# Kernel tuning notes

Measured on AMD Instinct MI355X. Metric: run time of the kernel, lower is better.

## Reference

```python
import jax, jax.numpy as jnp
import numpy as np

N_NODES = 50000
N_EDGES = 800000
HIDDEN = 128
N_REL = 64
NUM_HEADS = 8
HEAD_DIM = HIDDEN // NUM_HEADS


def setup_inputs() -> dict:
    key = jax.random.key(0)
    ks = jax.random.split(key, 20)
    s = 0.05
    inp = {
        "x": jax.random.normal(ks[0], (N_NODES, HIDDEN), dtype=jnp.float32),
        "timestamps": jax.random.uniform(ks[1], (N_NODES,), dtype=jnp.float32),
        "src": jax.random.randint(ks[2], (N_EDGES,), 0, N_NODES),
        "dst": jax.random.randint(ks[3], (N_EDGES,), 0, N_NODES),
        "edge_type": jax.random.randint(ks[4], (N_EDGES,), 0, N_REL),
        "edge_time": jax.random.uniform(ks[5], (N_EDGES,), dtype=jnp.float32),
        # parameters (torch Linear stored as [in, out] so we use x @ W + b)
        "rel_table": jax.random.normal(ks[6], (N_REL, HIDDEN), dtype=jnp.float32) * s,
        "Wq": jax.random.normal(ks[7], (HIDDEN, HIDDEN), dtype=jnp.float32) * s,
        "bq": jnp.zeros((HIDDEN,), dtype=jnp.float32),
        "Wk": jax.random.normal(ks[8], (HIDDEN, HIDDEN), dtype=jnp.float32) * s,
        "bk": jnp.zeros((HIDDEN,), dtype=jnp.float32),
        "Wv": jax.random.normal(ks[9], (HIDDEN, HIDDEN), dtype=jnp.float32) * s,
        "bv": jnp.zeros((HIDDEN,), dtype=jnp.float32),
        "W1": jax.random.normal(ks[10], (2 * HIDDEN + 1, HIDDEN), dtype=jnp.float32) * s,
        "b1": jnp.zeros((HIDDEN,), dtype=jnp.float32),
        "W2": jax.random.normal(ks[11], (HIDDEN, 1), dtype=jnp.float32) * s,
        "b2": jnp.zeros((1,), dtype=jnp.float32),
        "time_coeff": jnp.array(1.0, dtype=jnp.float32),
    }
    return inp


def reference(x, timestamps, src, dst, edge_type, edge_time, rel_table,
              Wq, bq, Wk, bk, Wv, bv, W1, b1, W2, b2, time_coeff):
    N = x.shape[0]
    # temporal gating
    delta_t = (timestamps[dst] - edge_time) / (jnp.abs(time_coeff) + 1e-9)  # [E]
    time_mask = jax.nn.sigmoid(delta_t)[:, None]                            # [E,1]
    rel_emb = rel_table[edge_type] * time_mask                              # [E,H]
    src_emb = x[src]                                                        # [E,H]
    # dynamic edge weights: MLP([src_emb, rel_emb, time_mask]) -> sigmoid
    weight_input = jnp.concatenate([src_emb, rel_emb, time_mask], axis=-1)  # [E,2H+1]
    h = jax.nn.relu(weight_input @ W1 + b1)
    dynamic_weights = jax.nn.sigmoid(h @ W2 + b2)                           # [E,1]
    message = src_emb * rel_emb * dynamic_weights                           # [E,H]
    # multi-head edge attention keyed by dst
    q = (x[dst] @ Wq + bq).reshape(-1, NUM_HEADS, HEAD_DIM)
    k = (message @ Wk + bk).reshape(-1, NUM_HEADS, HEAD_DIM)
    v = (message @ Wv + bv).reshape(-1, NUM_HEADS, HEAD_DIM)
    scores = (q * k).sum(-1) / (HEAD_DIM ** 0.5)                            # [E,heads]
    # scatter softmax over edges grouped by dst
    seg_max = jax.ops.segment_max(scores, dst, num_segments=N)              # [N,heads]
    e = jnp.exp(scores - seg_max[dst])
    denom = jax.ops.segment_sum(e, dst, num_segments=N)
    attn = e / denom[dst]                                                   # [E,heads]
    out = jax.ops.segment_sum(v * attn[..., None], dst, num_segments=N)     # [N,heads,hd]
    return out.reshape(N, NUM_HEADS * HEAD_DIM)
```

## Files before the change

### kernel.cpp

```cpp
#include <hip/hip_runtime.h>

typedef __bf16 v8bf __attribute__((ext_vector_type(8)));
typedef __bf16 v4bf __attribute__((ext_vector_type(4)));
typedef float  v4f  __attribute__((ext_vector_type(4)));

#define MFMA16x16x32 __builtin_amdgcn_mfma_f32_16x16x32_bf16

#define HIDDEN 128
#define NHEADS 8

__global__ __launch_bounds__(512) void prep_all(
    const float* __restrict__ rel, const float* __restrict__ W1,
    const float* __restrict__ Wk, const float* __restrict__ Wv,
    const float* __restrict__ W2, const int* __restrict__ dst,
    int* __restrict__ count,
    __bf16* __restrict__ mlppre, __bf16* __restrict__ relbf,
    __bf16* __restrict__ wswz, __bf16* __restrict__ w2bf,
    float* __restrict__ outz,
    const float* __restrict__ x, const float* __restrict__ Wq,
    const float* __restrict__ bq, const float* __restrict__ b1,
    __bf16* __restrict__ qbf, __bf16* __restrict__ hpre, __bf16* __restrict__ xbf,
    int N, int E, int hb, int zb, int nz4)
{
  __shared__ __bf16 X[32][136];
  const int b = blockIdx.x;
  if (b < 64) {
    __shared__ float rrow[128];
    const int j = threadIdx.x;
    if (j < 128) rrow[j] = rel[b*HIDDEN + j];
    __syncthreads();
    if (j < 128) {
      float acc = W1[256*HIDDEN + j];
      #pragma unroll 4
      for (int k=0;k<128;k++) acc += rrow[k]*W1[(128+k)*HIDDEN + j];
      mlppre[b*HIDDEN + j] = (__bf16)acc;
      relbf [b*HIDDEN + j] = (__bf16)rrow[j];
    }
    return;
  }
  if (b < 72) {
    int f = (b - 64)*512 + threadIdx.x;
    if (f < 128) w2bf[f] = (__bf16)W2[f];
    if (f >= 2*8*4*64) return;
    int lane = f & 63, kk = (f>>6)&3, c = (f>>8)&7, mat = f>>11;
    const float* W = mat ? Wv : Wk;
    int qq = lane>>4, nn = lane&15;
    v8bf o;
    #pragma unroll
    for (int j=0;j<8;j++) o[j] = (__bf16)W[(kk*32 + qq*8 + j)*HIDDEN + c*16 + nn];
    *(v8bf*)(wswz + (long)f*8) = o;
    return;
  }
  if (b < 72 + hb) {
    long i = (long)(b - 72)*512 + threadIdx.x;
    long e4 = i*4;
    if (e4 + 3 < E) {
      int4 d = *(const int4*)(dst + e4);
      atomicAdd(&count[d.x], 1);
      atomicAdd(&count[d.y], 1);
      atomicAdd(&count[d.z], 1);
      atomicAdd(&count[d.w], 1);
    } else {
      for (long e = e4; e < E; e++) atomicAdd(&count[dst[e]], 1);
    }
    return;
  }
  if (b < 72 + hb + zb) {
    int idx = (b - 72 - hb)*512 + threadIdx.x;
    if (idx < nz4) ((float4*)outz)[idx] = make_float4(0.f,0.f,0.f,0.f);
    return;
  }
  const int pb = b - (72 + hb + zb), npb = gridDim.x - (72 + hb + zb);
  const int tid = threadIdx.x;
  const int w = tid >> 6, l = tid & 63, qd = l >> 4, ln = l & 15;
  const int col = w*16 + ln;

  v8bf BQ[4], BH[4];
  #pragma unroll
  for (int kk=0; kk<4; kk++) {
    v8bf f, g;
    #pragma unroll
    for (int j=0;j<8;j++){
      f[j] = (__bf16)Wq[(kk*32 + qd*8 + j)*HIDDEN + col];
      g[j] = (__bf16)W1[(kk*32 + qd*8 + j)*HIDDEN + col];
    }
    BQ[kk] = f; BH[kk] = g;
  }
  const float bqv = bq[col], b1v = b1[col];

  const int s = tid >> 4, c8 = (tid & 15)*8;
  for (int n0 = pb*32; n0 < N; n0 += npb*32) {
    __syncthreads();
    int n = n0 + s;
    v8bf xv;
    if (n < N) {
      const float4* xp = (const float4*)(x + (long)n*HIDDEN + c8);
      float4 a = xp[0], b2_ = xp[1];
      xv[0]=(__bf16)a.x; xv[1]=(__bf16)a.y; xv[2]=(__bf16)a.z; xv[3]=(__bf16)a.w;
      xv[4]=(__bf16)b2_.x; xv[5]=(__bf16)b2_.y; xv[6]=(__bf16)b2_.z; xv[7]=(__bf16)b2_.w;
      *(v8bf*)(xbf + (long)n*HIDDEN + c8) = xv;
    } else {
      #pragma unroll
      for (int j=0;j<8;j++) xv[j] = (__bf16)0.f;
    }
    *(v8bf*)&X[s][c8] = xv;
    __syncthreads();

    v4f q0={0.f,0.f,0.f,0.f}, q1={0.f,0.f,0.f,0.f};
    v4f h0={0.f,0.f,0.f,0.f}, h1={0.f,0.f,0.f,0.f};
    #pragma unroll
    for (int kk=0;kk<4;kk++) {
      v8bf a0 = *(const v8bf*)&X[ln][kk*32 + qd*8];
      v8bf a1 = *(const v8bf*)&X[16+ln][kk*32 + qd*8];
      q0 = MFMA16x16x32(a0, BQ[kk], q0, 0,0,0);
      q1 = MFMA16x16x32(a1, BQ[kk], q1, 0,0,0);
      h0 = MFMA16x16x32(a0, BH[kk], h0, 0,0,0);
      h1 = MFMA16x16x32(a1, BH[kk], h1, 0,0,0);
    }
    #pragma unroll
    for (int r=0;r<4;r++) {
      int n_o = n0 + qd*4 + r;
      if (n_o < N) {
        qbf [(long)n_o*HIDDEN + col] = (__bf16)(q0[r] + bqv);
        hpre[(long)n_o*HIDDEN + col] = (__bf16)(h0[r] + b1v);
      }
      int n2 = n0 + 16 + qd*4 + r;
      if (n2 < N) {
        qbf [(long)n2*HIDDEN + col] = (__bf16)(q1[r] + bqv);
        hpre[(long)n2*HIDDEN + col] = (__bf16)(h1[r] + b1v);
      }
    }
  }
}

__global__ __launch_bounds__(1024) void scan_kernel(const int* __restrict__ count,
    int* __restrict__ base, int N)
{
  __shared__ int ssum[1024];
  const int t = threadIdx.x;
  const int chunk = ((N + 4095) >> 12) << 2;
  const int lo = t*chunk, hi = min(lo + chunk, N);
  int s = 0;
  int i = lo;
  for (; i + 3 < hi; i += 4) {
    int4 v = *(const int4*)(count + i);
    s += v.x + v.y + v.z + v.w;
  }
  for (; i < hi; i++) s += count[i];
  ssum[t] = s;
  __syncthreads();
  #pragma unroll
  for (int ofs = 1; ofs < 1024; ofs <<= 1) {
    int v = (t >= ofs) ? ssum[t - ofs] : 0;
    __syncthreads();
    ssum[t] += v;
    __syncthreads();
  }
  int run = (t == 0) ? 0 : ssum[t-1];
  i = lo;
  for (; i + 3 < hi; i += 4) {
    int4 c = *(const int4*)(count + i);
    int4 o;
    o.x = run; o.y = run + c.x; o.z = o.y + c.y; o.w = o.z + c.z;
    *(int4*)(base + i) = o;
    run = o.w + c.w;
  }
  for (; i < hi; i++) { base[i] = run; run += count[i]; }
}

__global__ __launch_bounds__(512) void scat_dw(
    const int* __restrict__ src, const int* __restrict__ dstp,
    const int* __restrict__ etyp, const float* __restrict__ etime,
    const float* __restrict__ ts, const float* __restrict__ tc,
    const __bf16* __restrict__ hpre, const __bf16* __restrict__ mlppre,
    const __bf16* __restrict__ w2bf, const float* __restrict__ b2,
    const int* __restrict__ base, int* __restrict__ cursor,
    int4* __restrict__ meta4, int E)
{
  const int tid = threadIdx.x;
  const int wid = tid >> 6, l = tid & 63;
  const long e0 = ((long)blockIdx.x*8 + wid)*8;
  const int ei = l >> 3, lc = l & 7;

  int s_=0, d_=0, ty_=0; float et_=0.f, tsd_=0.f;
  if (l < 8 && e0 + l < E) {
    long e = e0 + l;
    s_ = src[e]; d_ = dstp[e]; ty_ = etyp[e]; et_ = etime[e]; tsd_ = ts[d_];
  }
  const int sE  = __shfl(s_, ei);
  const int dE  = __shfl(d_, ei);
  const int tyE = __shfl(ty_, ei);
  const float etE  = __shfl(et_, ei);
  const float tsdE = __shfl(tsd_, ei);

  const float invtc = 1.0f / (fabsf(tc[0]) + 1e-9f);
  const float dt = (tsdE - etE) * invtc;
  const float tm = 1.0f/(1.0f + __expf(-dt));

  const v8bf w2a = *(const v8bf*)(w2bf + lc*16);
  const v8bf w2b = *(const v8bf*)(w2bf + lc*16 + 8);
  const __bf16* hp = hpre  + (long)sE *HIDDEN + lc*16;
  const __bf16* mp = mlppre+ (long)tyE*HIDDEN + lc*16;
  v8bf av0 = *(const v8bf*)hp, av1 = *(const v8bf*)(hp + 8);
  v8bf bp0 = *(const v8bf*)mp, bp1 = *(const v8bf*)(mp + 8);

  float z = 0.f;
  #pragma unroll
  for (int j=0;j<8;j++){
    float p0 = (float)av0[j] + tm*(float)bp0[j];
    float p1 = (float)av1[j] + tm*(float)bp1[j];
    z += fmaxf(p0, 0.f)*(float)w2a[j] + fmaxf(p1, 0.f)*(float)w2b[j];
  }
  z += __shfl_xor(z,1); z += __shfl_xor(z,2); z += __shfl_xor(z,4);

  if (lc == 0 && e0 + ei < E) {
    float dw = 1.0f/(1.0f + __expf(-(z + b2[0])));
    int p = base[dE] + atomicAdd(&cursor[dE], 1);
    meta4[p] = make_int4(sE, dE, tyE, __float_as_int(tm * dw));
  }
}

__global__ __launch_bounds__(512, 4) void edge_fused6(
    const int4* __restrict__ meta4,
    const __bf16* __restrict__ xbf, const __bf16* __restrict__ qbf,
    const __bf16* __restrict__ relbf, const __bf16* __restrict__ wswz,
    const float* __restrict__ bk, const float* __restrict__ bv,
    float* __restrict__ out, float* __restrict__ denom, int E, int ntiles)
{
  __shared__ __align__(16) __bf16 MSG[2][4096];

  const int tid = threadIdx.x;
  const int wid = tid >> 6, l = tid & 63, qd = l >> 4, ln = l & 15;
  const int eIdx = wid*4 + qd;

  v8bf bkf[4], bvf[4];
  #pragma unroll
  for (int kk=0;kk<4;kk++){
    bkf[kk] = *(const v8bf*)(wswz +         wid*2048 + kk*512 + (size_t)l*8);
    bvf[kk] = *(const v8bf*)(wswz + 16384 + wid*2048 + kk*512 + (size_t)l*8);
  }
  const float bkc = bk[wid*16 + ln];
  const float bvc = bv[wid*16 + ln];

  const int G = gridDim.x;
  const int wg = ((int)blockIdx.x & 7)*(G >> 3) + ((int)blockIdx.x >> 3);
  const int lo = (int)((long)wg*ntiles/G);
  const int hi = (int)((long)(wg+1)*ntiles/G);
  if (lo >= hi) return;

  int t = lo;
  int4 mt = make_int4(0, -1, 0, 0);
  { int e = t*32 + l; if (l < 32 && e < E) mt = meta4[e]; }
  int tn = t + 1;
  int4 mtn = make_int4(0, -1, 0, 0);
  if (tn < hi) { int e = tn*32 + l; if (l < 32 && e < E) mtn = meta4[e]; }

  float sME = __int_as_float(__shfl(mt.w, eIdx));
  v8bf sv, rv;
  {
    int srcE = __shfl(mt.x, eIdx);
    int tyE  = __shfl(mt.z, eIdx);
    sv = *(const v8bf*)(xbf   + (long)srcE*HIDDEN + ln*8);
    rv = *(const v8bf*)(relbf + (long)tyE *HIDDEN + ln*8);
  }
  int dC[2][4];
  #pragma unroll
  for (int b=0;b<2;b++)
    #pragma unroll
    for (int r=0;r<4;r++) dC[b][r] = __shfl(mt.y, b*16 + qd*4 + r);
  float qA[2][4];
  #pragma unroll
  for (int b=0;b<2;b++)
    #pragma unroll
    for (int r=0;r<4;r++){
      int d = dC[b][r];
      qA[b][r] = (float)qbf[(long)(d<0?0:d)*HIDDEN + wid*16 + ln];
    }

  int p = 0;
  while (true) {
    const int d_m = mt.y;

    int dprev = __shfl(d_m, (l>0)?(l-1):0);
    int flag = (l < 32) && ((l==0) || (d_m != dprev));
    unsigned long long segmask = __ballot(flag);

    const int t2 = tn + 1;
    int4 mt2 = make_int4(0, -1, 0, 0);
    if (t2 < hi) { int e = t2*32 + l; if (l < 32 && e < E) mt2 = meta4[e]; }

    const float sMN = __int_as_float(__shfl(mtn.w, eIdx));
    const int srcN = __shfl(mtn.x, eIdx);
    const int tyN  = __shfl(mtn.z, eIdx);
    int dN[2][4];
    #pragma unroll
    for (int b=0;b<2;b++)
      #pragma unroll
      for (int r=0;r<4;r++) dN[b][r] = __shfl(mtn.y, b*16 + qd*4 + r);

    {
      char* wbase = (char*)&MSG[p][0] + eIdx*256;
      const int sw = (eIdx & 7) << 4;
      v8bf m;
      #pragma unroll
      for (int j=0;j<8;j++) m[j] = (__bf16)((float)sv[j]*(float)rv[j]*sME);
      *(v8bf*)(wbase + ((ln*16) ^ sw)) = m;
    }

    sv = *(const v8bf*)(xbf   + (long)srcN*HIDDEN + ln*8);
    rv = *(const v8bf*)(relbf + (long)tyN *HIDDEN + ln*8);

    float qB[2][4];
    #pragma unroll
    for (int b=0;b<2;b++)
      #pragma unroll
      for (int r=0;r<4;r++){
        int d = dN[b][r];
        qB[b][r] = (float)qbf[(long)(d<0?0:d)*HIDDEN + wid*16 + ln];
      }

    asm volatile("s_waitcnt lgkmcnt(0)" ::: "memory");
    __builtin_amdgcn_s_barrier();
    __builtin_amdgcn_sched_barrier(0);

    const char* rb = (const char*)&MSG[p][0];
    v4f aK[2], aV[2];
    __builtin_amdgcn_s_setprio(1);
    #pragma unroll
    for (int b=0;b<2;b++){
      const int rrow = b*16 + ln;
      const char* abase = rb + rrow*256;
      const int asw = (rrow & 7) << 4;
      v4f k_ = {0.f,0.f,0.f,0.f}, v_ = {0.f,0.f,0.f,0.f};
      #pragma unroll
      for (int kk=0;kk<4;kk++){
        v8bf a = *(const v8bf*)(abase + ((kk*64 + qd*16) ^ asw));
        k_ = MFMA16x16x32(a, bkf[kk], k_, 0,0,0);
        v_ = MFMA16x16x32(a, bvf[kk], v_, 0,0,0);
      }
      aK[b] = k_; aV[b] = v_;
    }
    __builtin_amdgcn_s_setprio(0);

    float sc[2][4];
    #pragma unroll
    for (int b=0;b<2;b++)
      #pragma unroll
      for (int r=0;r<4;r++) sc[b][r] = (aK[b][r] + bkc)*qA[b][r];
    #pragma unroll
    for (int m=1;m<16;m<<=1){
      #pragma unroll
      for (int b=0;b<2;b++)
        #pragma unroll
        for (int r=0;r<4;r++) sc[b][r] += __shfl_xor(sc[b][r], m);
    }
    float ee[2][4], wv[2][4];
    #pragma unroll
    for (int b=0;b<2;b++)
      #pragma unroll
      for (int r=0;r<4;r++){
        float e_ = __expf(sc[b][r]*0.25f);
        ee[b][r] = e_;
        wv[b][r] = e_*(aV[b][r] + bvc);
      }

    unsigned long long mm = segmask;
    while (mm){
      int s0 = __ffsll((long long)mm) - 1;
      mm &= mm - 1;
      int s1 = mm ? (__ffsll((long long)mm) - 1) : 32;
      int dseg = __shfl(d_m, s0);
      if (dseg < 0) continue;
      float a0 = 0.f, dn0 = 0.f;
      #pragma unroll
      for (int b=0;b<2;b++)
        #pragma unroll
        for (int r=0;r<4;r++){
          int rw = b*16 + qd*4 + r;
          bool in = (rw >= s0) && (rw < s1);
          a0  += in ? wv[b][r] : 0.f;
          dn0 += in ? ee[b][r] : 0.f;
        }
      a0  += __shfl_xor(a0,16);  a0  += __shfl_xor(a0,32);
      dn0 += __shfl_xor(dn0,16); dn0 += __shfl_xor(dn0,32);
      if (l < 16) atomicAdd(&out[(long)dseg*HIDDEN + wid*16 + ln], a0);
      if (l == 0) atomicAdd(&denom[(long)dseg*NHEADS + wid], dn0);
    }

    if (tn >= hi) break;
    t = tn; tn = t2; mt = mtn; mtn = mt2; sME = sMN;
    #pragma unroll
    for (int b=0;b<2;b++)
      #pragma unroll
      for (int r=0;r<4;r++){
        dC[b][r] = dN[b][r];
        qA[b][r] = qB[b][r];
      }
    p ^= 1;
  }
}

__global__ __launch_bounds__(512) void q_kernel(const float* __restrict__ x,
    const float* __restrict__ Wq, const float* __restrict__ bq,
    float* __restrict__ q, int N)
{
  __shared__ __bf16 X[32][136];
  const int tid = threadIdx.x;
  const int w = tid >> 6, l = tid & 63, qd = l >> 4, ln = l & 15;
  const int col = w*16 + ln;
  v8bf B[4];
  #pragma unroll
  for (int kk=0; kk<4; kk++) {
    v8bf f;
    #pragma unroll
    for (int j=0;j<8;j++) f[j] = (__bf16)Wq[(kk*32 + qd*8 + j)*HIDDEN + col];
    B[kk] = f;
  }
  const float bqv = bq[col];
  const int s = tid >> 4, c8 = (tid & 15)*8;
  for (int n0 = blockIdx.x*32; n0 < N; n0 += gridDim.x*32) {
    __syncthreads();
    int n = n0 + s;
    v8bf xv;
    if (n < N) {
      const float4* xp = (const float4*)(x + (long)n*HIDDEN + c8);
      float4 a = xp[0], b = xp[1];
      xv[0]=(__bf16)a.x; xv[1]=(__bf16)a.y; xv[2]=(__bf16)a.z; xv[3]=(__bf16)a.w;
      xv[4]=(__bf16)b.x; xv[5]=(__bf16)b.y; xv[6]=(__bf16)b.z; xv[7]=(__bf16)b.w;
    } else {
      #pragma unroll
      for (int j=0;j<8;j++) xv[j] = (__bf16)0.f;
    }
    *(v8bf*)&X[s][c8] = xv;
    __syncthreads();
    v4f acc0 = {0.f,0.f,0.f,0.f}, acc1 = {0.f,0.f,0.f,0.f};
    #pragma unroll
    for (int kk=0;kk<4;kk++) {
      v8bf a0 = *(const v8bf*)&X[ln][kk*32 + qd*8];
      v8bf a1 = *(const v8bf*)&X[16+ln][kk*32 + qd*8];
      acc0 = MFMA16x16x32(a0, B[kk], acc0, 0,0,0);
      acc1 = MFMA16x16x32(a1, B[kk], acc1, 0,0,0);
    }
    #pragma unroll
    for (int r=0;r<4;r++) {
      int n_o = n0 + qd*4 + r;
      if (n_o < N) q[(long)n_o*HIDDEN + col] = acc0[r] + bqv;
      int n_o2 = n0 + 16 + qd*4 + r;
      if (n_o2 < N) q[(long)n_o2*HIDDEN + col] = acc1[r] + bqv;
    }
  }
}

__global__ __launch_bounds__(512) void edge_atomic(
    const float* __restrict__ x, const float* __restrict__ ts,
    const int* __restrict__ src, const int* __restrict__ dst,
    const int* __restrict__ etyp, const float* __restrict__ etime,
    const float* __restrict__ rel,
    const float* __restrict__ Wk, const float* __restrict__ bk,
    const float* __restrict__ Wv, const float* __restrict__ bv,
    const float* __restrict__ W1, const float* __restrict__ b1,
    const float* __restrict__ W2, const float* __restrict__ b2,
    const float* __restrict__ tc,
    const float* __restrict__ qws, float* __restrict__ denom,
    float* __restrict__ out, int E)
{
  __shared__ __bf16 A[32][264];
  __shared__ __bf16 A2[32][136];
  __shared__ float sW2[128], sb1[128], sw1r[128], sbk[128], sbv[128];
  __shared__ float stm[32], sdw[32];
  __shared__ int   ssrc[32], sdst[32], styp[32];
  __shared__ float dwpart[8][32];
  const int tid = threadIdx.x;
  const int w = tid >> 6, l = tid & 63, qd = l >> 4, ln = l & 15;
  const int col = w*16 + ln;
  v8bf B1[8], BK[4], BV[4];
  #pragma unroll
  for (int kk=0;kk<8;kk++){ v8bf f;
    #pragma unroll
    for (int j=0;j<8;j++) f[j] = (__bf16)W1[(kk*32+qd*8+j)*HIDDEN + col];
    B1[kk]=f; }
  #pragma unroll
  for (int kk=0;kk<4;kk++){ v8bf f,g;
    #pragma unroll
    for (int j=0;j<8;j++){ f[j] = (__bf16)Wk[(kk*32+qd*8+j)*HIDDEN + col];
                           g[j] = (__bf16)Wv[(kk*32+qd*8+j)*HIDDEN + col]; }
    BK[kk]=f; BV[kk]=g; }
  if (tid < 128) {
    sW2[tid]=W2[tid]; sb1[tid]=b1[tid]; sw1r[tid]=W1[256*HIDDEN+tid];
    sbk[tid]=bk[tid]; sbv[tid]=bv[tid];
  }
  const float b2v = b2[0];
  const float invtc = 1.0f / (fabsf(tc[0]) + 1e-9f);
  const int s = tid >> 4, c8 = (tid & 15)*8;
  const int ntiles = (E + 31) >> 5;
  for (int t = blockIdx.x; t < ntiles; t += gridDim.x) {
    const int e0 = t*32;
    __syncthreads();
    if (tid < 32) {
      int e = e0 + tid;
      if (e < E) {
        int d = dst[e];
        ssrc[tid]=src[e]; sdst[tid]=d; styp[tid]=etyp[e];
        float dt = (ts[d] - etime[e]) * invtc;
        stm[tid] = 1.0f/(1.0f+expf(-dt));
      } else { ssrc[tid]=0; sdst[tid]=0; styp[tid]=0; stm[tid]=0.f; }
    }
    __syncthreads();
    {
      const float tmv = stm[s];
      const float4* xp = (const float4*)(x + (long)ssrc[s]*HIDDEN + c8);
      float4 a = xp[0], b = xp[1];
      const float4* rp = (const float4*)(rel + (long)styp[s]*HIDDEN + c8);
      float4 ra = rp[0], rb = rp[1];
      v8bf sv, rv;
      sv[0]=(__bf16)a.x; sv[1]=(__bf16)a.y; sv[2]=(__bf16)a.z; sv[3]=(__bf16)a.w;
      sv[4]=(__bf16)b.x; sv[5]=(__bf16)b.y; sv[6]=(__bf16)b.z; sv[7]=(__bf16)b.w;
      rv[0]=(__bf16)(ra.x*tmv); rv[1]=(__bf16)(ra.y*tmv);
      rv[2]=(__bf16)(ra.z*tmv); rv[3]=(__bf16)(ra.w*tmv);
      rv[4]=(__bf16)(rb.x*tmv); rv[5]=(__bf16)(rb.y*tmv);
      rv[6]=(__bf16)(rb.z*tmv); rv[7]=(__bf16)(rb.w*tmv);
      *(v8bf*)&A[s][c8] = sv;
      *(v8bf*)&A[s][128 + c8] = rv;
    }
    __syncthreads();
    v4f acc0={0.f,0.f,0.f,0.f}, acc1={0.f,0.f,0.f,0.f};
    #pragma unroll
    for (int kk=0;kk<8;kk++){
      v8bf a0 = *(const v8bf*)&A[ln][kk*32 + qd*8];
      v8bf a1 = *(const v8bf*)&A[16+ln][kk*32 + qd*8];
      acc0 = MFMA16x16x32(a0, B1[kk], acc0, 0,0,0);
      acc1 = MFMA16x16x32(a1, B1[kk], acc1, 0,0,0);
    }
    float part[8];
    {
      const float w1rj = sw1r[col], b1j = sb1[col], w2j = sW2[col];
      #pragma unroll
      for (int r=0;r<4;r++){
        int i0 = qd*4 + r, i1 = 16 + qd*4 + r;
        part[r]   = fmaxf(acc0[r] + stm[i0]*w1rj + b1j, 0.f)*w2j;
        part[4+r] = fmaxf(acc1[r] + stm[i1]*w1rj + b1j, 0.f)*w2j;
      }
    }
    #pragma unroll
    for (int m=1;m<16;m<<=1){
      #pragma unroll
      for (int i=0;i<8;i++) part[i] += __shfl_xor(part[i], m, 16);
    }
    if (ln == 0){
      #pragma unroll
      for (int r=0;r<4;r++){ dwpart[w][qd*4+r]=part[r]; dwpart[w][16+qd*4+r]=part[4+r]; }
    }
    __syncthreads();
    if (tid < 32){
      float z = b2v;
      #pragma unroll
      for (int ww=0;ww<8;ww++) z += dwpart[ww][tid];
      sdw[tid] = 1.0f/(1.0f+expf(-z));
    }
    __syncthreads();
    {
      const float dwv = sdw[s];
      v8bf mv;
      #pragma unroll
      for (int i=0;i<8;i++)
        mv[i] = (__bf16)((float)A[s][c8+i]*(float)A[s][128+c8+i]*dwv);
      *(v8bf*)&A2[s][c8] = mv;
    }
    __syncthreads();
    v4f k0={0.f,0.f,0.f,0.f}, k1={0.f,0.f,0.f,0.f};
    v4f v0={0.f,0.f,0.f,0.f}, v1={0.f,0.f,0.f,0.f};
    #pragma unroll
    for (int kk=0;kk<4;kk++){
      v8bf a0 = *(const v8bf*)&A2[ln][kk*32 + qd*8];
      v8bf a1 = *(const v8bf*)&A2[16+ln][kk*32 + qd*8];
      k0 = MFMA16x16x32(a0, BK[kk], k0, 0,0,0);
      k1 = MFMA16x16x32(a1, BK[kk], k1, 0,0,0);
      v0 = MFMA16x16x32(a0, BV[kk], v0, 0,0,0);
      v1 = MFMA16x16x32(a1, BV[kk], v1, 0,0,0);
    }
    float sc[8];
    const float bkj = sbk[col], bvj = sbv[col];
    #pragma unroll
    for (int r=0;r<4;r++){
      int i0 = qd*4 + r, i1 = 16 + qd*4 + r;
      sc[r]   = (k0[r]+bkj)*qws[(long)sdst[i0]*HIDDEN + col];
      sc[4+r] = (k1[r]+bkj)*qws[(long)sdst[i1]*HIDDEN + col];
    }
    #pragma unroll
    for (int m=1;m<16;m<<=1){
      #pragma unroll
      for (int i=0;i<8;i++) sc[i] += __shfl_xor(sc[i], m, 16);
    }
    float ee[8];
    #pragma unroll
    for (int i=0;i<8;i++) ee[i] = expf(sc[i]*0.25f);
    if (ln == 0){
      #pragma unroll
      for (int r=0;r<4;r++){
        int i0 = qd*4 + r, i1 = 16 + qd*4 + r;
        if (e0+i0 < E) atomicAdd(&denom[(long)sdst[i0]*NHEADS + w], ee[r]);
        if (e0+i1 < E) atomicAdd(&denom[(long)sdst[i1]*NHEADS + w], ee[4+r]);
      }
    }
    #pragma unroll
    for (int r=0;r<4;r++){
      int i0 = qd*4 + r, i1 = 16 + qd*4 + r;
      if (e0+i0 < E) atomicAdd(&out[(long)sdst[i0]*HIDDEN + col], ee[r]*(v0[r]+bvj));
      if (e0+i1 < E) atomicAdd(&out[(long)sdst[i1]*HIDDEN + col], ee[4+r]*(v1[r]+bvj));
    }
  }
}

__global__ void fin_kernel(float* __restrict__ out, const float* __restrict__ denom, int N)
{
  int idx = blockIdx.x*blockDim.x + threadIdx.x;
  int total = N*32;
  if (idx < total){
    int n = idx >> 5;
    int h = (idx & 31) >> 2;
    float d = denom[n*8 + h];
    float inv = d > 0.f ? 1.0f/d : 0.f;
    float4* p = (float4*)out + idx;
    float4 v = *p;
    v.x*=inv; v.y*=inv; v.z*=inv; v.w*=inv;
    *p = v;
  }
}

static inline size_t align256(size_t v){ return (v + 255) & ~(size_t)255; }

extern "C" void kernel_launch(void* const* d_in, const int* in_sizes, int n_in,
                              void* d_out, int out_size, void* d_ws, size_t ws_size,
                              hipStream_t stream)
{
  const float* x      = (const float*)d_in[0];
  const float* ts     = (const float*)d_in[1];
  const int*   src    = (const int*)d_in[2];
  const int*   dstp   = (const int*)d_in[3];
  const int*   etyp   = (const int*)d_in[4];
  const float* etime  = (const float*)d_in[5];
  const float* rel    = (const float*)d_in[6];
  const float* Wq     = (const float*)d_in[7];
  const float* bq     = (const float*)d_in[8];
  const float* Wk     = (const float*)d_in[9];
  const float* bk     = (const float*)d_in[10];
  const float* Wv     = (const float*)d_in[11];
  const float* bv     = (const float*)d_in[12];
  const float* W1     = (const float*)d_in[13];
  const float* b1     = (const float*)d_in[14];
  const float* W2     = (const float*)d_in[15];
  const float* b2     = (const float*)d_in[16];
  const float* tc     = (const float*)d_in[17];
  float* out = (float*)d_out;

  const int N = in_sizes[0] / HIDDEN;
  const int E = in_sizes[2];

  char* ws = (char*)d_ws;
  size_t off = 0;
  __bf16* qbf    = (__bf16*)(ws + off); off += align256((size_t)N*HIDDEN*2);
  __bf16* hpre   = (__bf16*)(ws + off); off += align256((size_t)N*HIDDEN*2);
  __bf16* xbf    = (__bf16*)(ws + off); off += align256((size_t)N*HIDDEN*2);
  __bf16* relbf  = (__bf16*)(ws + off); off += align256((size_t)64*HIDDEN*2);
  __bf16* mlppre = (__bf16*)(ws + off); off += align256((size_t)64*HIDDEN*2);
  __bf16* w2bf   = (__bf16*)(ws + off); off += align256((size_t)HIDDEN*2);
  __bf16* wswz   = (__bf16*)(ws + off); off += align256((size_t)4096*8*2);
  size_t zoff = off;
  int*    countp = (int*)(ws + off);    off += align256((size_t)N*4);
  int*    cursor = (int*)(ws + off);    off += align256((size_t)N*4);
  float*  denom  = (float*)(ws + off);  off += align256((size_t)N*NHEADS*4);
  size_t zlen = off - zoff;
  int4*   meta4  = (int4*)(ws + off);   off += align256((size_t)E*16);
  int*    basep  = (int*)(ws + off);    off += align256((size_t)N*4);
  const size_t needed_fast = off;

  if (ws_size >= needed_fast) {
    hipMemsetAsync(ws + zoff, 0, zlen, stream);

    const int hb = (E + 2047)/2048;
    const int nz4 = N*32;
    const int zb = (nz4 + 511)/512;
    prep_all<<<72 + hb + zb + 1024, 512, 0, stream>>>(rel, W1, Wk, Wv, W2,
        dstp, countp, mlppre, relbf, wswz, w2bf, out,
        x, Wq, bq, b1, qbf, hpre, xbf, N, E, hb, zb, nz4);
    scan_kernel<<<1, 1024, 0, stream>>>(countp, basep, N);
    scat_dw<<<(E + 63)/64, 512, 0, stream>>>(src, dstp, etyp, etime, ts, tc,
        hpre, mlppre, w2bf, b2, basep, cursor, meta4, E);

    const int ntiles = (E + 31) >> 5;
    edge_fused6<<<2048, 512, 0, stream>>>(meta4,
        xbf, qbf, relbf, wswz, bk, bv, out, denom, E, ntiles);
    fin_kernel<<<(N*32 + 255)/256, 256, 0, stream>>>(out, denom, N);
  } else {
    float* qws    = (float*)ws;
    float* denom2 = (float*)(ws + align256((size_t)N*HIDDEN*4));
    hipMemsetAsync(out,    0, (size_t)N*HIDDEN*4, stream);
    hipMemsetAsync(denom2, 0, (size_t)N*NHEADS*4, stream);
    q_kernel<<<512, 512, 0, stream>>>(x, Wq, bq, qws, N);
    edge_atomic<<<512, 512, 0, stream>>>(x, ts, src, dstp, etyp, etime, rel,
        Wk, bk, Wv, bv, W1, b1, W2, b2, tc, qws, denom2, out, E);
    fin_kernel<<<(N*32 + 255)/256, 256, 0, stream>>>(out, denom2, N);
  }
}
```

Measured before the change: 454.6 us.

## Make each wave own a full edge tile, loop heads over LDS-resident weights

The edge kernel now loads the full swizzled Wk/Wv weights (64KB) into LDS once per block. Each wave processes an entire 32-edge tile on its own and loops over the 8 heads, keeping the message fragments in registers. This removes the per-tile LDS message exchange and the block-wide barrier, and it drops the software double-buffered meta prefetch in favour of a grid-stride loop. The 1/sqrt(d) scale is folded into Wk and bk. The trade-off is higher LDS use, serialized per-head atomics within one wave, and the loss of the explicit cross-tile load prefetch.

```diff
diff --git a/kernel.cpp b/kernel.cpp
--- a/kernel.cpp
+++ b/kernel.cpp
@@ -44,10 +44,11 @@
     if (f >= 2*8*4*64) return;
     int lane = f & 63, kk = (f>>6)&3, c = (f>>8)&7, mat = f>>11;
     const float* W = mat ? Wv : Wk;
+    const float scl = mat ? 1.0f : 0.25f;
     int qq = lane>>4, nn = lane&15;
     v8bf o;
     #pragma unroll
-    for (int j=0;j<8;j++) o[j] = (__bf16)W[(kk*32 + qq*8 + j)*HIDDEN + c*16 + nn];
+    for (int j=0;j<8;j++) o[j] = (__bf16)(W[(kk*32 + qq*8 + j)*HIDDEN + c*16 + nn]*scl);
     *(v8bf*)(wswz + (long)f*8) = o;
     return;
   }
@@ -220,183 +221,153 @@
   }
 }
 
-__global__ __launch_bounds__(512, 4) void edge_fused6(
+__global__ __launch_bounds__(512, 4) void edge_fused7(
     const int4* __restrict__ meta4,
     const __bf16* __restrict__ xbf, const __bf16* __restrict__ qbf,
     const __bf16* __restrict__ relbf, const __bf16* __restrict__ wswz,
     const float* __restrict__ bk, const float* __restrict__ bv,
     float* __restrict__ out, float* __restrict__ denom, int E, int ntiles)
 {
-  __shared__ __align__(16) __bf16 MSG[2][4096];
+  __shared__ __align__(16) __bf16 W[32768];
+  __shared__ float sbk[128], sbv[128];
 
   const int tid = threadIdx.x;
-  const int wid = tid >> 6, l = tid & 63, qd = l >> 4, ln = l & 15;
-  const int eIdx = wid*4 + qd;
-
-  v8bf bkf[4], bvf[4];
+  const int l = tid & 63, qd = l >> 4, ln = l & 15;
+
   #pragma unroll
-  for (int kk=0;kk<4;kk++){
-    bkf[kk] = *(const v8bf*)(wswz +         wid*2048 + kk*512 + (size_t)l*8);
-    bvf[kk] = *(const v8bf*)(wswz + 16384 + wid*2048 + kk*512 + (size_t)l*8);
-  }
-  const float bkc = bk[wid*16 + ln];
-  const float bvc = bv[wid*16 + ln];
-
-  const int G = gridDim.x;
-  const int wg = ((int)blockIdx.x & 7)*(G >> 3) + ((int)blockIdx.x >> 3);
-  const int lo = (int)((long)wg*ntiles/G);
-  const int hi = (int)((long)(wg+1)*ntiles/G);
-  if (lo >= hi) return;
-
-  int t = lo;
-  int4 mt = make_int4(0, -1, 0, 0);
-  { int e = t*32 + l; if (l < 32 && e < E) mt = meta4[e]; }
-  int tn = t + 1;
-  int4 mtn = make_int4(0, -1, 0, 0);
-  if (tn < hi) { int e = tn*32 + l; if (l < 32 && e < E) mtn = meta4[e]; }
-
-  float sME = __int_as_float(__shfl(mt.w, eIdx));
-  v8bf sv, rv;
-  {
-    int srcE = __shfl(mt.x, eIdx);
-    int tyE  = __shfl(mt.z, eIdx);
-    sv = *(const v8bf*)(xbf   + (long)srcE*HIDDEN + ln*8);
-    rv = *(const v8bf*)(relbf + (long)tyE *HIDDEN + ln*8);
-  }
-  int dC[2][4];
-  #pragma unroll
-  for (int b=0;b<2;b++)
-    #pragma unroll
-    for (int r=0;r<4;r++) dC[b][r] = __shfl(mt.y, b*16 + qd*4 + r);
-  float qA[2][4];
-  #pragma unroll
-  for (int b=0;b<2;b++)
-    #pragma unroll
-    for (int r=0;r<4;r++){
-      int d = dC[b][r];
-      qA[b][r] = (float)qbf[(long)(d<0?0:d)*HIDDEN + wid*16 + ln];
-    }
-
-  int p = 0;
-  while (true) {
+  for (int i=0;i<8;i++) {
+    int o = (i*512 + tid)*8;
+    *(v8bf*)&W[o] = *(const v8bf*)(wswz + o);
+  }
+  if (tid < 128) { sbk[tid] = bk[tid]*0.25f; sbv[tid] = bv[tid]; }
+  __syncthreads();
+
+  const int nwaves = gridDim.x * 8;
+  const int w0 = blockIdx.x*8 + (tid >> 6);
+
+  for (int t = w0; t < ntiles; t += nwaves) {
+    int4 mt = make_int4(0, -1, 0, 0);
+    { int e = t*32 + l; if (l < 32 && e < E) mt = meta4[e]; }
     const int d_m = mt.y;
 
     int dprev = __shfl(d_m, (l>0)?(l-1):0);
     int flag = (l < 32) && ((l==0) || (d_m != dprev));
     unsigned long long segmask = __ballot(flag);
 
-    const int t2 = tn + 1;
-    int4 mt2 = make_int4(0, -1, 0, 0);
-    if (t2 < hi) { int e = t2*32 + l; if (l < 32 && e < E) mt2 = meta4[e]; }
-
-    const float sMN = __int_as_float(__shfl(mtn.w, eIdx));
-    const int srcN = __shfl(mtn.x, eIdx);
-    const int tyN  = __shfl(mtn.z, eIdx);
-    int dN[2][4];
+    int dC[2][4];
     #pragma unroll
     for (int b=0;b<2;b++)
       #pragma unroll
-      for (int r=0;r<4;r++) dN[b][r] = __shfl(mtn.y, b*16 + qd*4 + r);
-
-    {
-      char* wbase = (char*)&MSG[p][0] + eIdx*256;
-      const int sw = (eIdx & 7) << 4;
-      v8bf m;
-      #pragma unroll
-      for (int j=0;j<8;j++) m[j] = (__bf16)((float)sv[j]*(float)rv[j]*sME);
-      *(v8bf*)(wbase + ((ln*16) ^ sw)) = m;
-    }
-
-    sv = *(const v8bf*)(xbf   + (long)srcN*HIDDEN + ln*8);
-    rv = *(const v8bf*)(relbf + (long)tyN *HIDDEN + ln*8);
-
-    float qB[2][4];
+      for (int r=0;r<4;r++) dC[b][r] = __shfl(d_m, b*16 + qd*4 + r);
+
+    v8bf msgf[2][4];
+    #pragma unroll
+    for (int b=0;b<2;b++){
+      const int srcE = __shfl(mt.x, b*16 + ln);
+      const int tyE  = __shfl(mt.z, b*16 + ln);
+      const float sM = __int_as_float(__shfl(mt.w, b*16 + ln));
+      const __bf16* xs = xbf   + (long)srcE*HIDDEN + qd*8;
+      const __bf16* rs = relbf + (long)tyE *HIDDEN + qd*8;
+      #pragma unroll
+      for (int kk=0;kk<4;kk++){
+        v8bf xv = *(const v8bf*)(xs + kk*32);
+        v8bf rv = *(const v8bf*)(rs + kk*32);
+        v8bf m;
+        #pragma unroll
+        for (int j=0;j<8;j++) m[j] = (__bf16)((float)xv[j]*(float)rv[j]*sM);
+        msgf[b][kk] = m;
+      }
+    }
+
+    float qv[2][4];
     #pragma unroll
     for (int b=0;b<2;b++)
       #pragma unroll
       for (int r=0;r<4;r++){
-        int d = dN[b][r];
-        qB[b][r] = (float)qbf[(long)(d<0?0:d)*HIDDEN + wid*16 + ln];
-      }
-
-    asm volatile("s_waitcnt lgkmcnt(0)" ::: "memory");
-    __builtin_amdgcn_s_barrier();
-    __builtin_amdgcn_sched_barrier(0);
-
-    const char* rb = (const char*)&MSG[p][0];
-    v4f aK[2], aV[2];
-    __builtin_amdgcn_s_setprio(1);
-    #pragma unroll
-    for (int b=0;b<2;b++){
-      const int rrow = b*16 + ln;
-      const char* abase = rb + rrow*256;
-      const int asw = (rrow & 7) << 4;
-      v4f k_ = {0.f,0.f,0.f,0.f}, v_ = {0.f,0.f,0.f,0.f};
+        int d = dC[b][r];
+        qv[b][r] = (float)qbf[(long)(d<0?0:d)*HIDDEN + ln];
+      }
+
+    #pragma unroll 1
+    for (int c=0;c<8;c++){
+      v4f aK0={0.f,0.f,0.f,0.f}, aK1={0.f,0.f,0.f,0.f};
+      v4f aV0={0.f,0.f,0.f,0.f}, aV1={0.f,0.f,0.f,0.f};
+      __builtin_amdgcn_s_setprio(1);
       #pragma unroll
       for (int kk=0;kk<4;kk++){
-        v8bf a = *(const v8bf*)(abase + ((kk*64 + qd*16) ^ asw));
-        k_ = MFMA16x16x32(a, bkf[kk], k_, 0,0,0);
-        v_ = MFMA16x16x32(a, bvf[kk], v_, 0,0,0);
-      }
-      aK[b] = k_; aV[b] = v_;
-    }
-    __builtin_amdgcn_s_setprio(0);
-
-    float sc[2][4];
-    #pragma unroll
-    for (int b=0;b<2;b++)
-      #pragma unroll
-      for (int r=0;r<4;r++) sc[b][r] = (aK[b][r] + bkc)*qA[b][r];
-    #pragma unroll
-    for (int m=1;m<16;m<<=1){
-      #pragma unroll
-      for (int b=0;b<2;b++)
+        v8bf bkf = *(const v8bf*)&W[        c*2048 + kk*512 + l*8];
+        v8bf bvf = *(const v8bf*)&W[16384 + c*2048 + kk*512 + l*8];
+        aK0 = MFMA16x16x32(msgf[0][kk], bkf, aK0, 0,0,0);
+        aV0 = MFMA16x16x32(msgf[0][kk], bvf, aV0, 0,0,0);
+        aK1 = MFMA16x16x32(msgf[1][kk], bkf, aK1, 0,0,0);
+        aV1 = MFMA16x16x32(msgf[1][kk], bvf, aV1, 0,0,0);
+      }
+      __builtin_amdgcn_s_setprio(0);
+
+      float qn[2][4];
+      if (c < 7) {
         #pragma unroll
-        for (int r=0;r<4;r++) sc[b][r] += __shfl_xor(sc[b][r], m);
-    }
-    float ee[2][4], wv[2][4];
-    #pragma unroll
-    for (int b=0;b<2;b++)
+        for (int b=0;b<2;b++)
+          #pragma unroll
+          for (int r=0;r<4;r++){
+            int d = dC[b][r];
+            qn[b][r] = (float)qbf[(long)(d<0?0:d)*HIDDEN + (c+1)*16 + ln];
+          }
+      }
+
+      const float bkc = sbk[c*16 + ln], bvc = sbv[c*16 + ln];
+      float sc[2][4];
       #pragma unroll
       for (int r=0;r<4;r++){
-        float e_ = __expf(sc[b][r]*0.25f);
-        ee[b][r] = e_;
-        wv[b][r] = e_*(aV[b][r] + bvc);
-      }
-
-    unsigned long long mm = segmask;
-    while (mm){
-      int s0 = __ffsll((long long)mm) - 1;
-      mm &= mm - 1;
-      int s1 = mm ? (__ffsll((long long)mm) - 1) : 32;
-      int dseg = __shfl(d_m, s0);
-      if (dseg < 0) continue;
-      float a0 = 0.f, dn0 = 0.f;
-      #pragma unroll
-      for (int b=0;b<2;b++)
+        sc[0][r] = (aK0[r] + bkc)*qv[0][r];
+        sc[1][r] = (aK1[r] + bkc)*qv[1][r];
+      }
+      #pragma unroll
+      for (int m=1;m<16;m<<=1){
         #pragma unroll
-        for (int r=0;r<4;r++){
-          int rw = b*16 + qd*4 + r;
-          bool in = (rw >= s0) && (rw < s1);
-          a0  += in ? wv[b][r] : 0.f;
-          dn0 += in ? ee[b][r] : 0.f;
-        }
-      a0  += __shfl_xor(a0,16);  a0  += __shfl_xor(a0,32);
-      dn0 += __shfl_xor(dn0,16); dn0 += __shfl_xor(dn0,32);
-      if (l < 16) atomicAdd(&out[(long)dseg*HIDDEN + wid*16 + ln], a0);
-      if (l == 0) atomicAdd(&denom[(long)dseg*NHEADS + wid], dn0);
-    }
-
-    if (tn >= hi) break;
-    t = tn; tn = t2; mt = mtn; mtn = mt2; sME = sMN;
-    #pragma unroll
-    for (int b=0;b<2;b++)
+        for (int b=0;b<2;b++)
+          #pragma unroll
+          for (int r=0;r<4;r++) sc[b][r] += __shfl_xor(sc[b][r], m);
+      }
+      float ee[2][4], wv[2][4];
       #pragma unroll
       for (int r=0;r<4;r++){
-        dC[b][r] = dN[b][r];
-        qA[b][r] = qB[b][r];
-      }
-    p ^= 1;
+        float e0_ = __expf(sc[0][r]);
+        float e1_ = __expf(sc[1][r]);
+        ee[0][r] = e0_; wv[0][r] = e0_*(aV0[r] + bvc);
+        ee[1][r] = e1_; wv[1][r] = e1_*(aV1[r] + bvc);
+      }
+
+      unsigned long long mm = segmask;
+      while (mm){
+        int s0 = __ffsll((long long)mm) - 1;
+        mm &= mm - 1;
+        int s1 = mm ? (__ffsll((long long)mm) - 1) : 32;
+        int dseg = __shfl(d_m, s0);
+        if (dseg < 0) continue;
+        float a0 = 0.f, dn0 = 0.f;
+        #pragma unroll
+        for (int b=0;b<2;b++)
+          #pragma unroll
+          for (int r=0;r<4;r++){
+            int rw = b*16 + qd*4 + r;
+            bool in = (rw >= s0) && (rw < s1);
+            a0  += in ? wv[b][r] : 0.f;
+            dn0 += in ? ee[b][r] : 0.f;
+          }
+        a0  += __shfl_xor(a0,16);  a0  += __shfl_xor(a0,32);
+        dn0 += __shfl_xor(dn0,16); dn0 += __shfl_xor(dn0,32);
+        if (l < 16) atomicAdd(&out[(long)dseg*HIDDEN + c*16 + ln], a0);
+        if (l == 0) atomicAdd(&denom[(long)dseg*NHEADS + c], dn0);
+      }
+
+      if (c < 7) {
+        #pragma unroll
+        for (int b=0;b<2;b++)
+          #pragma unroll
+          for (int r=0;r<4;r++) qv[b][r] = qn[b][r];
+      }
+    }
   }
 }
 
@@ -688,7 +659,7 @@
         hpre, mlppre, w2bf, b2, basep, cursor, meta4, E);
 
     const int ntiles = (E + 31) >> 5;
-    edge_fused6<<<2048, 512, 0, stream>>>(meta4,
+    edge_fused7<<<1024, 512, 0, stream>>>(meta4,
         xbf, qbf, relbf, wswz, bk, bv, out, denom, E, ntiles);
     fin_kernel<<<(N*32 + 255)/256, 256, 0, stream>>>(out, denom, N);
   } else {
```

New measurement: 494.7 us. +8.8%, slower.
